# Kernel optimization log

Measured on AMD Instinct MI355X. Metric: run time of the kernel, lower is better.

Reference implementation:

```python
import jax, jax.numpy as jnp
import numpy as np
import math

B, S, D = 2, 1024, 2048
H, HD, ROT = 16, 128, 64
LQ, LKV = 1024, 512
ED, E, TOPK = 1024, 8, 2
EPS = 1e-6

def _rms(x, w):
    return w * (x * jax.lax.rsqrt(jnp.mean(x * x, axis=-1, keepdims=True) + EPS))

def _rope(x, cos, sin):
    # x: [B,S,H,R]; pairs are (even, odd) lanes, complex multiply expanded
    x0, x1 = x[..., 0::2], x[..., 1::2]
    c = cos[None, :, None, :]
    s = sin[None, :, None, :]
    out = jnp.stack([x0 * c - x1 * s, x0 * s + x1 * c], axis=-1)
    return out.reshape(x.shape)

def setup_inputs() -> dict:
    key = jax.random.key(0)
    ks = jax.random.split(key, 32)
    def rn(k, shape, fan):
        return jax.random.normal(k, shape, jnp.float32) / math.sqrt(fan)
    # RoPE tables
    theta = 10000.0 ** (-np.arange(0, ROT, 2, dtype=np.float32) / ROT)
    ang = np.arange(S, dtype=np.float32)[:, None] * theta[None, :]
    inp = {
        'x': jax.random.normal(ks[0], (B, S, D), jnp.float32),
        'freqs_cos': jnp.asarray(np.cos(ang)),
        'freqs_sin': jnp.asarray(np.sin(ang)),
        'w_norm1': jnp.ones((D,), jnp.float32),
        'w_lq': rn(ks[1], (D, LQ), D),
        'w_lkv': rn(ks[2], (D, LKV), D),
        'w_q': rn(ks[3], (LQ, H * HD), LQ),
        'w_k': rn(ks[4], (LKV, H * HD), LKV),
        'w_v': rn(ks[5], (LKV, H * HD), LKV),
        'w_qr': rn(ks[6], (LQ, H * ROT), LQ),
        'b_qr': jnp.zeros((H * ROT,), jnp.float32),
        'w_kr': rn(ks[7], (D, H * ROT), D),
        'b_kr': jnp.zeros((H * ROT,), jnp.float32),
        'w_o': rn(ks[8], (H * HD, D), H * HD),
        'b_o': jnp.zeros((D,), jnp.float32),
        'w_norm2': jnp.ones((D,), jnp.float32),
        'w_moe_norm': jnp.ones((D,), jnp.float32),
        'centroids': jax.random.normal(ks[9], (E, D), jnp.float32),
        'ws1': rn(ks[10], (D, ED), D),
        'bs1': jnp.zeros((ED,), jnp.float32),
        'ws2': rn(ks[11], (ED, D), ED),
        'bs2': jnp.zeros((D,), jnp.float32),
        'wr1': rn(ks[12], (E, D, ED), D),
        'br1': jnp.zeros((E, ED), jnp.float32),
        'wr2': rn(ks[13], (E, ED, D), ED),
        'br2': jnp.zeros((E, D), jnp.float32),
    }
    return inp

def reference(x, freqs_cos, freqs_sin, w_norm1, w_lq, w_lkv, w_q, w_k, w_v,
              w_qr, b_qr, w_kr, b_kr, w_o, b_o, w_norm2, w_moe_norm,
              centroids, ws1, bs1, ws2, bs2, wr1, br1, wr2, br2):
    # --- MLA attention with residual ---
    h = _rms(x, w_norm1)
    cq = h @ w_lq                      # [B,S,LQ]
    ckv = h @ w_lkv                    # [B,S,LKV]
    q = (cq @ w_q).reshape(B, S, H, HD)
    qr = _rope((cq @ w_qr + b_qr).reshape(B, S, H, ROT), freqs_cos, freqs_sin)
    k = (ckv @ w_k).reshape(B, S, H, HD)
    kr = _rope((h @ w_kr + b_kr).reshape(B, S, H, ROT), freqs_cos, freqs_sin)
    v = (ckv @ w_v).reshape(B, S, H, HD)
    qc = jnp.concatenate([q, qr], axis=-1)   # [B,S,H,HD+ROT]
    kc = jnp.concatenate([k, kr], axis=-1)
    scores = jnp.einsum('bqhd,bkhd->bhqk', qc, kc) / math.sqrt(HD + ROT)
    att = jax.nn.softmax(scores, axis=-1)
    o = jnp.einsum('bhqk,bkhd->bqhd', att, v).reshape(B, S, H * HD)
    x = x + (o @ w_o + b_o)
    # --- DeepSeekMoE (double RMSNorm per source) ---
    hn = _rms(_rms(x, w_norm2), w_moe_norm)
    shared = jax.nn.gelu((hn @ ws1 + bs1) @ ws2 + bs2, approximate=False)
    t = hn.reshape(-1, D)                      # [T,D], T=B*S
    aff = jax.nn.softmax(t @ centroids.T, axis=-1)  # [T,E]
    sc, idx = jax.lax.top_k(aff, TOPK)
    mask = jnp.zeros_like(aff).at[jnp.arange(t.shape[0])[:, None], idx].set(sc)
    mid = jnp.einsum('td,edf->tef', t, wr1) + br1          # [T,E,ED]
    out_e = jax.nn.gelu(jnp.einsum('tef,efd->ted', mid, wr2) + br2,
                        approximate=False)                  # [T,E,D]
    routed = jnp.einsum('te,ted->td', mask, out_e).reshape(B, S, D)
    return x + (hn + shared + routed)
```

## Files before the change

kernel.cpp:

```cpp
#include <hip/hip_runtime.h>
#include <math.h>

#define TT   2048
#define DM   2048
#define SEQ  1024
#define NH   16
#define NE   8
#define MB_  (1024*1024)
#define ATT_SCALE 0.07216878364870322f

typedef unsigned short u16;
typedef __attribute__((ext_vector_type(8))) short s8v;
typedef __attribute__((ext_vector_type(4))) float f4v;

__device__ __forceinline__ u16 f2bf(float f) {
  unsigned u = __builtin_bit_cast(unsigned, f);
  unsigned r = (u + 0x7fffu + ((u >> 16) & 1u)) >> 16;
  return (u16)r;
}
__device__ __forceinline__ float bf2f(u16 h) {
  return __builtin_bit_cast(float, (unsigned)h << 16);
}
__device__ __forceinline__ float gelu_f(float x) {
  return 0.5f * x * (1.0f + erff(x * 0.7071067811865476f));
}
__device__ __forceinline__ f4v mfma16(s8v a, s8v b, f4v c) {
  return __builtin_amdgcn_mfma_f32_16x16x32_bf16(a, b, c, 0, 0, 0);
}

__global__ __launch_bounds__(256) void tcast_k(const float* __restrict__ src,
                                               u16* __restrict__ dst, int R, int C) {
  __shared__ float tile[32][33];
  const size_t bofs = (size_t)blockIdx.z * R * C;
  src += bofs; dst += bofs;
  const int r0 = blockIdx.y * 32, c0 = blockIdx.x * 32;
  const int t = threadIdx.x;
  const int tr = t >> 3, tc4 = (t & 7) * 4;
  float4 v = *(const float4*)&src[(size_t)(r0 + tr) * C + c0 + tc4];
  tile[tr][tc4 + 0] = v.x; tile[tr][tc4 + 1] = v.y;
  tile[tr][tc4 + 2] = v.z; tile[tr][tc4 + 3] = v.w;
  __syncthreads();
  ushort4 o;
  o.x = f2bf(tile[tc4 + 0][tr]);
  o.y = f2bf(tile[tc4 + 1][tr]);
  o.z = f2bf(tile[tc4 + 2][tr]);
  o.w = f2bf(tile[tc4 + 3][tr]);
  *(ushort4*)&dst[(size_t)(c0 + tr) * R + r0 + tc4] = o;
}

__device__ __forceinline__ float block_sum(float v, float* red) {
#pragma unroll
  for (int m = 32; m; m >>= 1) v += __shfl_xor(v, m);
  __syncthreads();
  if ((threadIdx.x & 63) == 0) red[threadIdx.x >> 6] = v;
  __syncthreads();
  return red[0] + red[1] + red[2] + red[3];
}

__global__ __launch_bounds__(256) void rmsb_k(const float* __restrict__ x,
                                              const float* __restrict__ w,
                                              u16* __restrict__ out) {
  __shared__ float red[4];
  const int t = blockIdx.x, tid = threadIdx.x;
  const float* xr = x + (size_t)t * DM;
  float4 v0 = *(const float4*)&xr[tid * 4];
  float4 v1 = *(const float4*)&xr[1024 + tid * 4];
  float ss = v0.x*v0.x + v0.y*v0.y + v0.z*v0.z + v0.w*v0.w
           + v1.x*v1.x + v1.y*v1.y + v1.z*v1.z + v1.w*v1.w;
  float s = block_sum(ss, red);
  float r = rsqrtf(s * (1.0f / DM) + 1e-6f);
  float4 w0 = *(const float4*)&w[tid * 4];
  float4 w1 = *(const float4*)&w[1024 + tid * 4];
  u16* orow = out + (size_t)t * DM;
  ushort4 o0, o1;
  o0.x = f2bf(v0.x*r*w0.x); o0.y = f2bf(v0.y*r*w0.y);
  o0.z = f2bf(v0.z*r*w0.z); o0.w = f2bf(v0.w*r*w0.w);
  o1.x = f2bf(v1.x*r*w1.x); o1.y = f2bf(v1.y*r*w1.y);
  o1.z = f2bf(v1.z*r*w1.z); o1.w = f2bf(v1.w*r*w1.w);
  *(ushort4*)&orow[tid * 4] = o0;
  *(ushort4*)&orow[1024 + tid * 4] = o1;
}

__global__ __launch_bounds__(256) void rms2_k(const float* __restrict__ x,
                                              const float* __restrict__ w2,
                                              const float* __restrict__ wm,
                                              float* __restrict__ outf,
                                              u16* __restrict__ outb) {
  __shared__ float red[4];
  const int t = blockIdx.x, tid = threadIdx.x;
  const float* xr = x + (size_t)t * DM;
  float4 v0 = *(const float4*)&xr[tid * 4];
  float4 v1 = *(const float4*)&xr[1024 + tid * 4];
  float ss = v0.x*v0.x + v0.y*v0.y + v0.z*v0.z + v0.w*v0.w
           + v1.x*v1.x + v1.y*v1.y + v1.z*v1.z + v1.w*v1.w;
  float s1 = block_sum(ss, red);
  float r1 = rsqrtf(s1 * (1.0f / DM) + 1e-6f);
  float4 a0 = *(const float4*)&w2[tid * 4];
  float4 a1 = *(const float4*)&w2[1024 + tid * 4];
  float4 y0 = make_float4(v0.x*r1*a0.x, v0.y*r1*a0.y, v0.z*r1*a0.z, v0.w*r1*a0.w);
  float4 y1 = make_float4(v1.x*r1*a1.x, v1.y*r1*a1.y, v1.z*r1*a1.z, v1.w*r1*a1.w);
  float ss2 = y0.x*y0.x + y0.y*y0.y + y0.z*y0.z + y0.w*y0.w
            + y1.x*y1.x + y1.y*y1.y + y1.z*y1.z + y1.w*y1.w;
  float s2 = block_sum(ss2, red);
  float r2 = rsqrtf(s2 * (1.0f / DM) + 1e-6f);
  float4 b0 = *(const float4*)&wm[tid * 4];
  float4 b1 = *(const float4*)&wm[1024 + tid * 4];
  float4 z0 = make_float4(y0.x*r2*b0.x, y0.y*r2*b0.y, y0.z*r2*b0.z, y0.w*r2*b0.w);
  float4 z1 = make_float4(y1.x*r2*b1.x, y1.y*r2*b1.y, y1.z*r2*b1.z, y1.w*r2*b1.w);
  float* orow = outf + (size_t)t * DM;
  *(float4*)&orow[tid * 4] = z0;
  *(float4*)&orow[1024 + tid * 4] = z1;
  u16* brow = outb + (size_t)t * DM;
  ushort4 o0, o1;
  o0.x = f2bf(z0.x); o0.y = f2bf(z0.y); o0.z = f2bf(z0.z); o0.w = f2bf(z0.w);
  o1.x = f2bf(z1.x); o1.y = f2bf(z1.y); o1.z = f2bf(z1.z); o1.w = f2bf(z1.w);
  *(ushort4*)&brow[tid * 4] = o0;
  *(ushort4*)&brow[1024 + tid * 4] = o1;
}

template <int ACT, bool BIAS, bool RES, int OUT>
__global__ __launch_bounds__(256) void bgemm_k(const u16* __restrict__ A, int lda,
                                               const u16* __restrict__ Bt, int ldb,
                                               void* __restrict__ C, int ldc, int K,
                                               const float* __restrict__ bias,
                                               const float* __restrict__ res, int ldr) {
  __shared__ u16 As[128 * 64];
  __shared__ u16 Bs[128 * 64];
  const int tid = threadIdx.x;
  const int lane = tid & 63, w = tid >> 6;
  const int wr = w >> 1, wc = w & 1;
  const int l15 = lane & 15, l4 = lane >> 4;
  const int bm = blockIdx.y * 128, bn = blockIdx.x * 128;
  int srow[4], ssw[4], scol[4];
#pragma unroll
  for (int i = 0; i < 4; ++i) {
    int q = i * 256 + tid;
    int row = q >> 3, c = q & 7;
    srow[i] = row; scol[i] = c * 8;
    ssw[i] = row * 64 + ((c ^ (row & 7)) * 8);
  }
  f4v acc[4][4] = {};
  for (int k0 = 0; k0 < K; k0 += 64) {
    s8v ra[4], rb[4];
#pragma unroll
    for (int i = 0; i < 4; ++i) {
      ra[i] = *(const s8v*)(A + (size_t)(bm + srow[i]) * lda + k0 + scol[i]);
      rb[i] = *(const s8v*)(Bt + (size_t)(bn + srow[i]) * ldb + k0 + scol[i]);
    }
    __syncthreads();
#pragma unroll
    for (int i = 0; i < 4; ++i) {
      *(s8v*)(As + ssw[i]) = ra[i];
      *(s8v*)(Bs + ssw[i]) = rb[i];
    }
    __syncthreads();
#pragma unroll
    for (int kk = 0; kk < 2; ++kk) {
      s8v af[4], bfr[4];
#pragma unroll
      for (int m = 0; m < 4; ++m) {
        int row = wr * 64 + m * 16 + l15;
        int c = kk * 4 + l4;
        af[m] = *(const s8v*)(As + row * 64 + ((c ^ (row & 7)) * 8));
      }
#pragma unroll
      for (int n = 0; n < 4; ++n) {
        int row = wc * 64 + n * 16 + l15;
        int c = kk * 4 + l4;
        bfr[n] = *(const s8v*)(Bs + row * 64 + ((c ^ (row & 7)) * 8));
      }
#pragma unroll
      for (int m = 0; m < 4; ++m)
#pragma unroll
        for (int n = 0; n < 4; ++n)
          acc[m][n] = mfma16(af[m], bfr[n], acc[m][n]);
    }
  }
#pragma unroll
  for (int m = 0; m < 4; ++m) {
    const int row0 = bm + wr * 64 + m * 16 + l4 * 4;
#pragma unroll
    for (int n = 0; n < 4; ++n) {
      const int col = bn + wc * 64 + n * 16 + l15;
      f4v v = acc[m][n];
      float bv = BIAS ? bias[col] : 0.0f;
      if (OUT == 2) {
        ushort4 o;
        o.x = f2bf(v[0] + bv); o.y = f2bf(v[1] + bv);
        o.z = f2bf(v[2] + bv); o.w = f2bf(v[3] + bv);
        *(ushort4*)((u16*)C + (size_t)col * ldc + row0) = o;
      } else {
#pragma unroll
        for (int r = 0; r < 4; ++r) {
          float o = v[r] + bv;
          if (RES) o += res[(size_t)(row0 + r) * ldr + col];
          if (ACT == 1) o = gelu_f(o);
          if (OUT == 1) ((u16*)C)[(size_t)(row0 + r) * ldc + col] = f2bf(o);
          else          ((float*)C)[(size_t)(row0 + r) * ldc + col] = o;
        }
      }
    }
  }
}

template <bool GATHER, int ACT>
__global__ __launch_bounds__(256) void bgemm_grp_k(const u16* __restrict__ A, int lda,
                                                   const u16* __restrict__ BtAll, int K, int N,
                                                   u16* __restrict__ C,
                                                   const float* __restrict__ biasAll,
                                                   const int* __restrict__ counts,
                                                   const int* __restrict__ bases,
                                                   const int* __restrict__ entry_token) {
  const int e = blockIdx.z;
  const int cnt = counts[e];
  const int m0 = blockIdx.y * 128;
  if (m0 >= cnt) return;
  const int base = bases[e];
  const u16* Bt = BtAll + (size_t)e * K * N;
  const float* bias = biasAll + (size_t)e * N;
  __shared__ u16 As[128 * 64];
  __shared__ u16 Bs[128 * 64];
  const int tid = threadIdx.x;
  const int lane = tid & 63, w = tid >> 6;
  const int wr = w >> 1, wc = w & 1;
  const int l15 = lane & 15, l4 = lane >> 4;
  const int bn = blockIdx.x * 128;
  int arow[4], srow[4], ssw[4], scol[4];
#pragma unroll
  for (int i = 0; i < 4; ++i) {
    int q = i * 256 + tid;
    int row = q >> 3, c = q & 7;
    srow[i] = row; scol[i] = c * 8;
    ssw[i] = row * 64 + ((c ^ (row & 7)) * 8);
    int rr = m0 + row; if (rr >= cnt) rr = cnt - 1;
    arow[i] = GATHER ? entry_token[base + rr] : (base + rr);
  }
  f4v acc[4][4] = {};
  for (int k0 = 0; k0 < K; k0 += 64) {
    s8v ra[4], rb[4];
#pragma unroll
    for (int i = 0; i < 4; ++i) {
      ra[i] = *(const s8v*)(A + (size_t)arow[i] * lda + k0 + scol[i]);
      rb[i] = *(const s8v*)(Bt + (size_t)(bn + srow[i]) * K + k0 + scol[i]);
    }
    __syncthreads();
#pragma unroll
    for (int i = 0; i < 4; ++i) {
      *(s8v*)(As + ssw[i]) = ra[i];
      *(s8v*)(Bs + ssw[i]) = rb[i];
    }
    __syncthreads();
#pragma unroll
    for (int kk = 0; kk < 2; ++kk) {
      s8v af[4], bfr[4];
#pragma unroll
      for (int m = 0; m < 4; ++m) {
        int row = wr * 64 + m * 16 + l15;
        int c = kk * 4 + l4;
        af[m] = *(const s8v*)(As + row * 64 + ((c ^ (row & 7)) * 8));
      }
#pragma unroll
      for (int n = 0; n < 4; ++n) {
        int row = wc * 64 + n * 16 + l15;
        int c = kk * 4 + l4;
        bfr[n] = *(const s8v*)(Bs + row * 64 + ((c ^ (row & 7)) * 8));
      }
#pragma unroll
      for (int m = 0; m < 4; ++m)
#pragma unroll
        for (int n = 0; n < 4; ++n)
          acc[m][n] = mfma16(af[m], bfr[n], acc[m][n]);
    }
  }
#pragma unroll
  for (int m = 0; m < 4; ++m) {
    const int rl0 = m0 + wr * 64 + m * 16 + l4 * 4;
#pragma unroll
    for (int n = 0; n < 4; ++n) {
      const int col = bn + wc * 64 + n * 16 + l15;
      f4v v = acc[m][n];
      float bv = bias[col];
#pragma unroll
      for (int r = 0; r < 4; ++r) {
        const int rl = rl0 + r;
        if (rl < cnt) {
          float o = v[r] + bv;
          if (ACT == 1) o = gelu_f(o);
          C[(size_t)(base + rl) * N + col] = f2bf(o);
        }
      }
    }
  }
}

__global__ __launch_bounds__(256) void ropeb_k(u16* __restrict__ buf,
                                               const float* __restrict__ cosb,
                                               const float* __restrict__ sinb) {
  const int i = blockIdx.x * 256 + threadIdx.x;
  const int t = i >> 9;
  const int rem = i & 511;
  const int hh2 = rem >> 5, p = rem & 31;
  const int s = t & (SEQ - 1);
  const float c = cosb[s * 32 + p], sn = sinb[s * 32 + p];
  unsigned* ptr = (unsigned*)(buf + (size_t)t * 1024 + hh2 * 64 + p * 2);
  unsigned vv = *ptr;
  float x0 = bf2f((u16)(vv & 0xffffu)), x1 = bf2f((u16)(vv >> 16));
  float y0 = x0 * c - x1 * sn, y1 = x0 * sn + x1 * c;
  *ptr = (unsigned)f2bf(y0) | ((unsigned)f2bf(y1) << 16);
}

__global__ __launch_bounds__(256) void attnb_k(const u16* __restrict__ qb,
                                               const u16* __restrict__ qrb,
                                               const u16* __restrict__ kb,
                                               const u16* __restrict__ krb,
                                               const u16* __restrict__ vt,
                                               u16* __restrict__ ob) {
  __shared__ u16 Ks[32 * 200];
  __shared__ u16 Vs[128 * 40];
  __shared__ u16 Ps[4][16 * 40];
  const int tid = threadIdx.x, lane = tid & 63, w = tid >> 6;
  const int l15 = lane & 15, l4 = lane >> 4;
  const int hh = blockIdx.y, bb = blockIdx.z;
  const int tbase = bb * SEQ;
  const int q0 = blockIdx.x * 64 + w * 16;
  const int qtok = tbase + q0 + l15;
  s8v aq[6];
#pragma unroll
  for (int kc = 0; kc < 4; ++kc)
    aq[kc] = *(const s8v*)(qb + (size_t)qtok * 2048 + hh * 128 + kc * 32 + l4 * 8);
#pragma unroll
  for (int kc = 0; kc < 2; ++kc)
    aq[4 + kc] = *(const s8v*)(qrb + (size_t)qtok * 1024 + hh * 64 + kc * 32 + l4 * 8);
  f4v o[8] = {};
  float m_run[4] = {-1e30f, -1e30f, -1e30f, -1e30f};
  float l_run[4] = {0.f, 0.f, 0.f, 0.f};
  for (int kt = 0; kt < SEQ / 32; ++kt) {
    __syncthreads();
#pragma unroll
    for (int i = 0; i < 3; ++i) {
      int q = i * 256 + tid;
      int row = q / 24, c = q % 24;
      int tok = tbase + kt * 32 + row;
      s8v v;
      if (c < 16) v = *(const s8v*)(kb  + (size_t)tok * 2048 + hh * 128 + c * 8);
      else        v = *(const s8v*)(krb + (size_t)tok * 1024 + hh * 64 + (c - 16) * 8);
      *(s8v*)(Ks + row * 200 + c * 8) = v;
    }
#pragma unroll
    for (int i = 0; i < 2; ++i) {
      int q = i * 256 + tid;
      int row = q >> 2, c = q & 3;
      s8v v = *(const s8v*)(vt + (size_t)(hh * 128 + row) * 2048 + tbase + kt * 32 + c * 8);
      *(s8v*)(Vs + row * 40 + c * 8) = v;
    }
    __syncthreads();
    f4v s0 = {}, s1 = {};
#pragma unroll
    for (int kc = 0; kc < 6; ++kc) {
      s8v bk0 = *(const s8v*)(Ks + l15 * 200 + kc * 32 + l4 * 8);
      s8v bk1 = *(const s8v*)(Ks + (16 + l15) * 200 + kc * 32 + l4 * 8);
      s0 = mfma16(aq[kc], bk0, s0);
      s1 = mfma16(aq[kc], bk1, s1);
    }
    float scf[4];
#pragma unroll
    for (int r = 0; r < 4; ++r) {
      float a = s0[r] * ATT_SCALE, b = s1[r] * ATT_SCALE;
      float mt = fmaxf(a, b);
#pragma unroll
      for (int msk = 1; msk < 16; msk <<= 1) mt = fmaxf(mt, __shfl_xor(mt, msk));
      float mn = fmaxf(m_run[r], mt);
      float p0 = __expf(a - mn), p1 = __expf(b - mn);
      float rs = p0 + p1;
#pragma unroll
      for (int msk = 1; msk < 16; msk <<= 1) rs += __shfl_xor(rs, msk);
      float sc = __expf(m_run[r] - mn);
      l_run[r] = l_run[r] * sc + rs;
      m_run[r] = mn;
      scf[r] = sc;
      int rq = l4 * 4 + r;
      Ps[w][rq * 40 + l15] = f2bf(p0);
      Ps[w][rq * 40 + 16 + l15] = f2bf(p1);
    }
#pragma unroll
    for (int dt = 0; dt < 8; ++dt) {
      o[dt][0] *= scf[0]; o[dt][1] *= scf[1];
      o[dt][2] *= scf[2]; o[dt][3] *= scf[3];
    }
    s8v pa = *(const s8v*)(&Ps[w][l15 * 40 + l4 * 8]);
#pragma unroll
    for (int dt = 0; dt < 8; ++dt) {
      s8v bv = *(const s8v*)(Vs + (dt * 16 + l15) * 40 + l4 * 8);
      o[dt] = mfma16(pa, bv, o[dt]);
    }
  }
  float linv[4];
#pragma unroll
  for (int r = 0; r < 4; ++r) linv[r] = 1.0f / l_run[r];
#pragma unroll
  for (int dt = 0; dt < 8; ++dt)
#pragma unroll
    for (int r = 0; r < 4; ++r)
      ob[(size_t)(tbase + q0 + l4 * 4 + r) * 2048 + hh * 128 + dt * 16 + l15] =
          f2bf(o[dt][r] * linv[r]);
}

__global__ __launch_bounds__(256) void router_k(const float* __restrict__ hn,
                                                const float* __restrict__ cent,
                                                int* __restrict__ topk_idx,
                                                float* __restrict__ topk_w,
                                                int* __restrict__ pos,
                                                int* __restrict__ counts) {
  const int t = blockIdx.x, tid = threadIdx.x;
  float p[NE] = {};
  const float* xr = hn + (size_t)t * DM;
  for (int d = tid * 4; d < DM; d += 1024) {
    float4 xv = *(const float4*)&xr[d];
#pragma unroll
    for (int e = 0; e < NE; ++e) {
      float4 cv = *(const float4*)&cent[e * DM + d];
      p[e] += xv.x * cv.x + xv.y * cv.y + xv.z * cv.z + xv.w * cv.w;
    }
  }
  __shared__ float wred[NE][4];
#pragma unroll
  for (int e = 0; e < NE; ++e) {
    float v = p[e];
#pragma unroll
    for (int m = 32; m; m >>= 1) v += __shfl_xor(v, m);
    if ((tid & 63) == 0) wred[e][tid >> 6] = v;
  }
  __syncthreads();
  if (tid == 0) {
    float lg[NE], mx = -3.0e38f;
    for (int e = 0; e < NE; ++e) {
      lg[e] = wred[e][0] + wred[e][1] + wred[e][2] + wred[e][3];
      mx = fmaxf(mx, lg[e]);
    }
    float pe[NE], sum = 0.f;
    for (int e = 0; e < NE; ++e) { pe[e] = expf(lg[e] - mx); sum += pe[e]; }
    const float inv = 1.f / sum;
    int i0 = 0; float v0 = -1.f;
    for (int e = 0; e < NE; ++e) { float a = pe[e] * inv; if (a > v0) { v0 = a; i0 = e; } }
    int i1 = 0; float v1 = -1.f;
    for (int e = 0; e < NE; ++e) { if (e == i0) continue; float a = pe[e] * inv; if (a > v1) { v1 = a; i1 = e; } }
    topk_idx[t * 2 + 0] = i0;
    topk_idx[t * 2 + 1] = i1;
    topk_w[t * 2 + 0] = v0;
    topk_w[t * 2 + 1] = v1;
    pos[t * 2 + 0] = atomicAdd(&counts[i0], 1);
    pos[t * 2 + 1] = atomicAdd(&counts[i1], 1);
  }
}

__global__ __launch_bounds__(256) void scatter_k(const int* __restrict__ topk_idx,
                                                 const int* __restrict__ pos,
                                                 const int* __restrict__ counts,
                                                 int* __restrict__ bases,
                                                 int* __restrict__ entry_token,
                                                 int* __restrict__ token_entry) {
  __shared__ int sb[NE];
  const int tid = threadIdx.x;
  if (tid == 0) {
    int acc = 0;
    for (int e = 0; e < NE; ++e) { sb[e] = acc; bases[e] = acc; acc += counts[e]; }
  }
  __syncthreads();
  for (int i = tid; i < TT * 2; i += 256) {
    const int e = topk_idx[i];
    const int entry = sb[e] + pos[i];
    entry_token[entry] = i >> 1;
    token_entry[i] = entry;
  }
}

__global__ __launch_bounds__(256) void combine_k(const float* __restrict__ x2,
                                                 const float* __restrict__ hn,
                                                 const float* __restrict__ sh,
                                                 const u16* __restrict__ oute,
                                                 const int* __restrict__ token_entry,
                                                 const float* __restrict__ topk_w,
                                                 float* __restrict__ out) {
  const int i = blockIdx.x * 256 + threadIdx.x;
  const int t = i >> 9;
  const int c = (i & 511) * 4;
  const int e0 = token_entry[t * 2 + 0], e1 = token_entry[t * 2 + 1];
  const float w0 = topk_w[t * 2 + 0], w1 = topk_w[t * 2 + 1];
  float4 a = *(const float4*)&x2[(size_t)t * DM + c];
  float4 b = *(const float4*)&hn[(size_t)t * DM + c];
  float4 s = *(const float4*)&sh[(size_t)t * DM + c];
  ushort4 u0 = *(const ushort4*)&oute[(size_t)e0 * DM + c];
  ushort4 u1 = *(const ushort4*)&oute[(size_t)e1 * DM + c];
  *(float4*)&out[(size_t)t * DM + c] =
      make_float4(a.x + b.x + s.x + w0 * bf2f(u0.x) + w1 * bf2f(u1.x),
                  a.y + b.y + s.y + w0 * bf2f(u0.y) + w1 * bf2f(u1.y),
                  a.z + b.z + s.z + w0 * bf2f(u0.z) + w1 * bf2f(u1.z),
                  a.w + b.w + s.w + w0 * bf2f(u0.w) + w1 * bf2f(u1.w));
}

extern "C" void kernel_launch(void* const* d_in, const int* in_sizes, int n_in,
                              void* d_out, int out_size, void* d_ws, size_t ws_size,
                              hipStream_t stream) {
  (void)in_sizes; (void)n_in; (void)out_size; (void)ws_size;
  const float* x       = (const float*)d_in[0];
  const float* fc      = (const float*)d_in[1];
  const float* fs      = (const float*)d_in[2];
  const float* w_norm1 = (const float*)d_in[3];
  const float* w_lq    = (const float*)d_in[4];
  const float* w_lkv   = (const float*)d_in[5];
  const float* w_q     = (const float*)d_in[6];
  const float* w_k     = (const float*)d_in[7];
  const float* w_v     = (const float*)d_in[8];
  const float* w_qr    = (const float*)d_in[9];
  const float* b_qr    = (const float*)d_in[10];
  const float* w_kr    = (const float*)d_in[11];
  const float* b_kr    = (const float*)d_in[12];
  const float* w_o     = (const float*)d_in[13];
  const float* b_o     = (const float*)d_in[14];
  const float* w_norm2 = (const float*)d_in[15];
  const float* w_moe   = (const float*)d_in[16];
  const float* cent    = (const float*)d_in[17];
  const float* ws1     = (const float*)d_in[18];
  const float* bs1     = (const float*)d_in[19];
  const float* ws2     = (const float*)d_in[20];
  const float* bs2     = (const float*)d_in[21];
  const float* wr1     = (const float*)d_in[22];
  const float* br1     = (const float*)d_in[23];
  const float* wr2     = (const float*)d_in[24];
  const float* br2     = (const float*)d_in[25];
  float* out = (float*)d_out;

  char* W = (char*)d_ws;
  u16* wt_lq  = (u16*)(W + (size_t)0  * MB_);
  u16* wt_lkv = (u16*)(W + (size_t)4  * MB_);
  u16* wt_q   = (u16*)(W + (size_t)6  * MB_);
  u16* wt_qr  = (u16*)(W + (size_t)10 * MB_);
  u16* wt_k   = (u16*)(W + (size_t)12 * MB_);
  u16* wt_kr  = (u16*)(W + (size_t)14 * MB_);
  u16* wt_v   = (u16*)(W + (size_t)18 * MB_);
  u16* wt_o   = (u16*)(W + (size_t)20 * MB_);
  u16* wt_s1  = (u16*)(W + (size_t)28 * MB_);
  u16* wt_s2  = (u16*)(W + (size_t)32 * MB_);
  u16* wt_r1  = (u16*)(W + (size_t)36 * MB_);
  u16* wt_r2  = (u16*)(W + (size_t)68 * MB_);
  u16* h_bf   = (u16*)(W + (size_t)100 * MB_);
  u16* cq_bf  = (u16*)(W + (size_t)108 * MB_);
  u16* ckv_bf = (u16*)(W + (size_t)112 * MB_);
  u16* qbuf   = (u16*)(W + (size_t)114 * MB_);
  u16* qrbuf  = (u16*)(W + (size_t)122 * MB_);
  u16* kbuf   = (u16*)(W + (size_t)126 * MB_);
  u16* krbuf  = (u16*)(W + (size_t)134 * MB_);
  u16* vbuf_t = (u16*)(W + (size_t)138 * MB_);
  u16* obuf   = (u16*)(W + (size_t)146 * MB_);
  float* x2   = (float*)(W + (size_t)100 * MB_);
  float* hn   = (float*)(W + (size_t)116 * MB_);
  u16* hn_bf  = (u16*)(W + (size_t)132 * MB_);
  u16* s1b    = (u16*)(W + (size_t)140 * MB_);
  float* shb  = (float*)(W + (size_t)144 * MB_);
  u16* midb   = (u16*)(W + (size_t)160 * MB_);
  u16* oute   = (u16*)(W + (size_t)168 * MB_);
  int* ip          = (int*)(W + (size_t)184 * MB_);
  int* counts      = ip;
  int* bases       = ip + 8;
  int* topk_idx    = ip + 16;
  int* pos         = ip + 16 + 4096;
  int* token_entry = ip + 16 + 8192;
  int* entry_token = ip + 16 + 12288;
  float* topk_w    = (float*)(ip + 16 + 16384);

  tcast_k<<<dim3(32, 64), 256, 0, stream>>>(w_lq,  wt_lq,  2048, 1024);
  tcast_k<<<dim3(16, 64), 256, 0, stream>>>(w_lkv, wt_lkv, 2048, 512);
  tcast_k<<<dim3(64, 32), 256, 0, stream>>>(w_q,   wt_q,   1024, 2048);
  tcast_k<<<dim3(32, 32), 256, 0, stream>>>(w_qr,  wt_qr,  1024, 1024);
  tcast_k<<<dim3(64, 16), 256, 0, stream>>>(w_k,   wt_k,   512,  2048);
  tcast_k<<<dim3(32, 64), 256, 0, stream>>>(w_kr,  wt_kr,  2048, 1024);
  tcast_k<<<dim3(64, 16), 256, 0, stream>>>(w_v,   wt_v,   512,  2048);
  tcast_k<<<dim3(64, 64), 256, 0, stream>>>(w_o,   wt_o,   2048, 2048);
  tcast_k<<<dim3(32, 64), 256, 0, stream>>>(ws1,   wt_s1,  2048, 1024);
  tcast_k<<<dim3(64, 32), 256, 0, stream>>>(ws2,   wt_s2,  1024, 2048);
  tcast_k<<<dim3(32, 64, 8), 256, 0, stream>>>(wr1, wt_r1, 2048, 1024);
  tcast_k<<<dim3(64, 32, 8), 256, 0, stream>>>(wr2, wt_r2, 1024, 2048);

  rmsb_k<<<TT, 256, 0, stream>>>(x, w_norm1, h_bf);
  bgemm_k<0, false, false, 1><<<dim3(8, 16), 256, 0, stream>>>(h_bf, 2048, wt_lq, 2048, cq_bf, 1024, 2048, nullptr, nullptr, 0);
  bgemm_k<0, false, false, 1><<<dim3(4, 16), 256, 0, stream>>>(h_bf, 2048, wt_lkv, 2048, ckv_bf, 512, 2048, nullptr, nullptr, 0);
  bgemm_k<0, false, false, 1><<<dim3(16, 16), 256, 0, stream>>>(cq_bf, 1024, wt_q, 1024, qbuf, 2048, 1024, nullptr, nullptr, 0);
  bgemm_k<0, true,  false, 1><<<dim3(8, 16), 256, 0, stream>>>(cq_bf, 1024, wt_qr, 1024, qrbuf, 1024, 1024, b_qr, nullptr, 0);
  bgemm_k<0, false, false, 1><<<dim3(16, 16), 256, 0, stream>>>(ckv_bf, 512, wt_k, 512, kbuf, 2048, 512, nullptr, nullptr, 0);
  bgemm_k<0, true,  false, 1><<<dim3(8, 16), 256, 0, stream>>>(h_bf, 2048, wt_kr, 2048, krbuf, 1024, 2048, b_kr, nullptr, 0);
  bgemm_k<0, false, false, 2><<<dim3(16, 16), 256, 0, stream>>>(ckv_bf, 512, wt_v, 512, vbuf_t, 2048, 512, nullptr, nullptr, 0);
  ropeb_k<<<4096, 256, 0, stream>>>(qrbuf, fc, fs);
  ropeb_k<<<4096, 256, 0, stream>>>(krbuf, fc, fs);
  attnb_k<<<dim3(16, NH, 2), 256, 0, stream>>>(qbuf, qrbuf, kbuf, krbuf, vbuf_t, obuf);
  bgemm_k<0, true, true, 0><<<dim3(16, 16), 256, 0, stream>>>(obuf, 2048, wt_o, 2048, x2, 2048, 2048, b_o, x, 2048);
  rms2_k<<<TT, 256, 0, stream>>>(x2, w_norm2, w_moe, hn, hn_bf);
  bgemm_k<0, true, false, 1><<<dim3(8, 16), 256, 0, stream>>>(hn_bf, 2048, wt_s1, 2048, s1b, 1024, 2048, bs1, nullptr, 0);
  bgemm_k<1, true, false, 0><<<dim3(16, 16), 256, 0, stream>>>(s1b, 1024, wt_s2, 1024, shb, 2048, 1024, bs2, nullptr, 0);
  hipMemsetAsync(counts, 0, NE * sizeof(int), stream);
  router_k<<<TT, 256, 0, stream>>>(hn, cent, topk_idx, topk_w, pos, counts);
  scatter_k<<<1, 256, 0, stream>>>(topk_idx, pos, counts, bases, entry_token, token_entry);
  bgemm_grp_k<true, 0><<<dim3(8, 32, NE), 256, 0, stream>>>(hn_bf, 2048, wt_r1, 2048, 1024, midb, br1, counts, bases, entry_token);
  bgemm_grp_k<false, 1><<<dim3(16, 32, NE), 256, 0, stream>>>(midb, 1024, wt_r2, 1024, 2048, oute, br2, counts, bases, nullptr);
  combine_k<<<4096, 256, 0, stream>>>(x2, hn, shb, oute, token_entry, topk_w, out);
}
```

Measured before the change: 905.0 us.

## Fuse attention projection GEMMs and load GEMM tiles directly into LDS

The separate projections that share an input are merged into wider GEMMs by concatenating transposed weights: lq, lkv and kr share one GEMM on h, q and qr share one on cq, and k and v share one on ckv, with v written transposed through a split epilogue. Bias vectors are packed into combined buffers by a small fill kernel. GEMM operand tiles are now staged with global_load_lds, bypassing registers, and the XOR swizzle on the LDS layout is dropped. Launch count and tail waves drop, but the unswizzled LDS reads may cause bank conflicts, and loads are still not double-buffered.

```diff
diff --git a/kernel.cpp b/kernel.cpp
--- a/kernel.cpp
+++ b/kernel.cpp
@@ -26,6 +26,11 @@
 }
 __device__ __forceinline__ f4v mfma16(s8v a, s8v b, f4v c) {
   return __builtin_amdgcn_mfma_f32_16x16x32_bf16(a, b, c, 0, 0, 0);
+}
+__device__ __forceinline__ void gload16(const u16* g, u16* l) {
+  __builtin_amdgcn_global_load_lds(
+      (const __attribute__((address_space(1))) unsigned*)g,
+      (__attribute__((address_space(3))) unsigned*)l, 16, 0, 0);
 }
 
 __global__ __launch_bounds__(256) void tcast_k(const float* __restrict__ src,
@@ -46,6 +51,15 @@
   o.z = f2bf(tile[tc4 + 2][tr]);
   o.w = f2bf(tile[tc4 + 3][tr]);
   *(ushort4*)&dst[(size_t)(c0 + tr) * R + r0 + tc4] = o;
+}
+
+__global__ __launch_bounds__(256) void biasfill_k(float* __restrict__ bh,
+                                                  float* __restrict__ bq,
+                                                  const float* __restrict__ bkr,
+                                                  const float* __restrict__ bqr) {
+  const int i = blockIdx.x * 256 + threadIdx.x;
+  if (i < 2560) bh[i] = (i >= 1536) ? bkr[i - 1536] : 0.f;
+  bq[i] = (i >= 2048) ? bqr[i - 2048] : 0.f;
 }
 
 __device__ __forceinline__ float block_sum(float v, float* red) {
@@ -123,7 +137,8 @@
                                                const u16* __restrict__ Bt, int ldb,
                                                void* __restrict__ C, int ldc, int K,
                                                const float* __restrict__ bias,
-                                               const float* __restrict__ res, int ldr) {
+                                               const float* __restrict__ res, int ldr,
+                                               void* __restrict__ C2, int ldc2, int nsplit) {
   __shared__ u16 As[128 * 64];
   __shared__ u16 Bs[128 * 64];
   const int tid = threadIdx.x;
@@ -131,44 +146,29 @@
   const int wr = w >> 1, wc = w & 1;
   const int l15 = lane & 15, l4 = lane >> 4;
   const int bm = blockIdx.y * 128, bn = blockIdx.x * 128;
-  int srow[4], ssw[4], scol[4];
-#pragma unroll
-  for (int i = 0; i < 4; ++i) {
-    int q = i * 256 + tid;
-    int row = q >> 3, c = q & 7;
-    srow[i] = row; scol[i] = c * 8;
-    ssw[i] = row * 64 + ((c ^ (row & 7)) * 8);
-  }
+  const int lrow = lane >> 3, lcol = (lane & 7) * 8;
+  const u16* Abase = A + (size_t)(bm + w * 32 + lrow) * lda + lcol;
+  const u16* Bbase = Bt + (size_t)(bn + w * 32 + lrow) * ldb + lcol;
+  u16* AsW = As + (w * 32) * 64;
+  u16* BsW = Bs + (w * 32) * 64;
   f4v acc[4][4] = {};
   for (int k0 = 0; k0 < K; k0 += 64) {
-    s8v ra[4], rb[4];
-#pragma unroll
-    for (int i = 0; i < 4; ++i) {
-      ra[i] = *(const s8v*)(A + (size_t)(bm + srow[i]) * lda + k0 + scol[i]);
-      rb[i] = *(const s8v*)(Bt + (size_t)(bn + srow[i]) * ldb + k0 + scol[i]);
-    }
     __syncthreads();
 #pragma unroll
-    for (int i = 0; i < 4; ++i) {
-      *(s8v*)(As + ssw[i]) = ra[i];
-      *(s8v*)(Bs + ssw[i]) = rb[i];
+    for (int j = 0; j < 4; ++j) {
+      gload16(Abase + (size_t)j * 8 * lda + k0, AsW + j * 8 * 64);
+      gload16(Bbase + (size_t)j * 8 * ldb + k0, BsW + j * 8 * 64);
     }
     __syncthreads();
 #pragma unroll
     for (int kk = 0; kk < 2; ++kk) {
       s8v af[4], bfr[4];
 #pragma unroll
-      for (int m = 0; m < 4; ++m) {
-        int row = wr * 64 + m * 16 + l15;
-        int c = kk * 4 + l4;
-        af[m] = *(const s8v*)(As + row * 64 + ((c ^ (row & 7)) * 8));
-      }
-#pragma unroll
-      for (int n = 0; n < 4; ++n) {
-        int row = wc * 64 + n * 16 + l15;
-        int c = kk * 4 + l4;
-        bfr[n] = *(const s8v*)(Bs + row * 64 + ((c ^ (row & 7)) * 8));
-      }
+      for (int m = 0; m < 4; ++m)
+        af[m] = *(const s8v*)(As + (wr * 64 + m * 16 + l15) * 64 + kk * 32 + l4 * 8);
+#pragma unroll
+      for (int n = 0; n < 4; ++n)
+        bfr[n] = *(const s8v*)(Bs + (wc * 64 + n * 16 + l15) * 64 + kk * 32 + l4 * 8);
 #pragma unroll
       for (int m = 0; m < 4; ++m)
 #pragma unroll
@@ -184,19 +184,19 @@
       const int col = bn + wc * 64 + n * 16 + l15;
       f4v v = acc[m][n];
       float bv = BIAS ? bias[col] : 0.0f;
-      if (OUT == 2) {
+      if (OUT == 3 && col >= nsplit) {
         ushort4 o;
         o.x = f2bf(v[0] + bv); o.y = f2bf(v[1] + bv);
         o.z = f2bf(v[2] + bv); o.w = f2bf(v[3] + bv);
-        *(ushort4*)((u16*)C + (size_t)col * ldc + row0) = o;
+        *(ushort4*)((u16*)C2 + (size_t)(col - nsplit) * ldc2 + row0) = o;
       } else {
 #pragma unroll
         for (int r = 0; r < 4; ++r) {
           float o = v[r] + bv;
           if (RES) o += res[(size_t)(row0 + r) * ldr + col];
           if (ACT == 1) o = gelu_f(o);
-          if (OUT == 1) ((u16*)C)[(size_t)(row0 + r) * ldc + col] = f2bf(o);
-          else          ((float*)C)[(size_t)(row0 + r) * ldc + col] = o;
+          if (OUT == 0) ((float*)C)[(size_t)(row0 + r) * ldc + col] = o;
+          else          ((u16*)C)[(size_t)(row0 + r) * ldc + col] = f2bf(o);
         }
       }
     }
@@ -225,46 +225,35 @@
   const int wr = w >> 1, wc = w & 1;
   const int l15 = lane & 15, l4 = lane >> 4;
   const int bn = blockIdx.x * 128;
-  int arow[4], srow[4], ssw[4], scol[4];
-#pragma unroll
-  for (int i = 0; i < 4; ++i) {
-    int q = i * 256 + tid;
-    int row = q >> 3, c = q & 7;
-    srow[i] = row; scol[i] = c * 8;
-    ssw[i] = row * 64 + ((c ^ (row & 7)) * 8);
-    int rr = m0 + row; if (rr >= cnt) rr = cnt - 1;
-    arow[i] = GATHER ? entry_token[base + rr] : (base + rr);
-  }
+  const int lrow = lane >> 3, lcol = (lane & 7) * 8;
+  int aro[4];
+#pragma unroll
+  for (int j = 0; j < 4; ++j) {
+    int rr = m0 + w * 32 + j * 8 + lrow;
+    if (rr >= cnt) rr = cnt - 1;
+    aro[j] = GATHER ? entry_token[base + rr] : (base + rr);
+  }
+  const u16* Bbase = Bt + (size_t)(bn + w * 32 + lrow) * K + lcol;
+  u16* AsW = As + (w * 32) * 64;
+  u16* BsW = Bs + (w * 32) * 64;
   f4v acc[4][4] = {};
   for (int k0 = 0; k0 < K; k0 += 64) {
-    s8v ra[4], rb[4];
-#pragma unroll
-    for (int i = 0; i < 4; ++i) {
-      ra[i] = *(const s8v*)(A + (size_t)arow[i] * lda + k0 + scol[i]);
-      rb[i] = *(const s8v*)(Bt + (size_t)(bn + srow[i]) * K + k0 + scol[i]);
-    }
     __syncthreads();
 #pragma unroll
-    for (int i = 0; i < 4; ++i) {
-      *(s8v*)(As + ssw[i]) = ra[i];
-      *(s8v*)(Bs + ssw[i]) = rb[i];
+    for (int j = 0; j < 4; ++j) {
+      gload16(A + (size_t)aro[j] * lda + k0 + lcol, AsW + j * 8 * 64);
+      gload16(Bbase + (size_t)j * 8 * K + k0, BsW + j * 8 * 64);
     }
     __syncthreads();
 #pragma unroll
     for (int kk = 0; kk < 2; ++kk) {
       s8v af[4], bfr[4];
 #pragma unroll
-      for (int m = 0; m < 4; ++m) {
-        int row = wr * 64 + m * 16 + l15;
-        int c = kk * 4 + l4;
-        af[m] = *(const s8v*)(As + row * 64 + ((c ^ (row & 7)) * 8));
-      }
-#pragma unroll
-      for (int n = 0; n < 4; ++n) {
-        int row = wc * 64 + n * 16 + l15;
-        int c = kk * 4 + l4;
-        bfr[n] = *(const s8v*)(Bs + row * 64 + ((c ^ (row & 7)) * 8));
-      }
+      for (int m = 0; m < 4; ++m)
+        af[m] = *(const s8v*)(As + (wr * 64 + m * 16 + l15) * 64 + kk * 32 + l4 * 8);
+#pragma unroll
+      for (int n = 0; n < 4; ++n)
+        bfr[n] = *(const s8v*)(Bs + (wc * 64 + n * 16 + l15) * 64 + kk * 32 + l4 * 8);
 #pragma unroll
       for (int m = 0; m < 4; ++m)
 #pragma unroll
@@ -293,7 +282,7 @@
   }
 }
 
-__global__ __launch_bounds__(256) void ropeb_k(u16* __restrict__ buf,
+__global__ __launch_bounds__(256) void ropeb_k(u16* __restrict__ buf, int ldb,
                                                const float* __restrict__ cosb,
                                                const float* __restrict__ sinb) {
   const int i = blockIdx.x * 256 + threadIdx.x;
@@ -302,17 +291,17 @@
   const int hh2 = rem >> 5, p = rem & 31;
   const int s = t & (SEQ - 1);
   const float c = cosb[s * 32 + p], sn = sinb[s * 32 + p];
-  unsigned* ptr = (unsigned*)(buf + (size_t)t * 1024 + hh2 * 64 + p * 2);
+  unsigned* ptr = (unsigned*)(buf + (size_t)t * ldb + hh2 * 64 + p * 2);
   unsigned vv = *ptr;
   float x0 = bf2f((u16)(vv & 0xffffu)), x1 = bf2f((u16)(vv >> 16));
   float y0 = x0 * c - x1 * sn, y1 = x0 * sn + x1 * c;
   *ptr = (unsigned)f2bf(y0) | ((unsigned)f2bf(y1) << 16);
 }
 
-__global__ __launch_bounds__(256) void attnb_k(const u16* __restrict__ qb,
-                                               const u16* __restrict__ qrb,
-                                               const u16* __restrict__ kb,
-                                               const u16* __restrict__ krb,
+__global__ __launch_bounds__(256) void attnb_k(const u16* __restrict__ qb, int ldq,
+                                               const u16* __restrict__ qrb, int ldqr,
+                                               const u16* __restrict__ kb, int ldk,
+                                               const u16* __restrict__ krb, int ldkr,
                                                const u16* __restrict__ vt,
                                                u16* __restrict__ ob) {
   __shared__ u16 Ks[32 * 200];
@@ -327,10 +316,10 @@
   s8v aq[6];
 #pragma unroll
   for (int kc = 0; kc < 4; ++kc)
-    aq[kc] = *(const s8v*)(qb + (size_t)qtok * 2048 + hh * 128 + kc * 32 + l4 * 8);
+    aq[kc] = *(const s8v*)(qb + (size_t)qtok * ldq + hh * 128 + kc * 32 + l4 * 8);
 #pragma unroll
   for (int kc = 0; kc < 2; ++kc)
-    aq[4 + kc] = *(const s8v*)(qrb + (size_t)qtok * 1024 + hh * 64 + kc * 32 + l4 * 8);
+    aq[4 + kc] = *(const s8v*)(qrb + (size_t)qtok * ldqr + hh * 64 + kc * 32 + l4 * 8);
   f4v o[8] = {};
   float m_run[4] = {-1e30f, -1e30f, -1e30f, -1e30f};
   float l_run[4] = {0.f, 0.f, 0.f, 0.f};
@@ -342,8 +331,8 @@
       int row = q / 24, c = q % 24;
       int tok = tbase + kt * 32 + row;
       s8v v;
-      if (c < 16) v = *(const s8v*)(kb  + (size_t)tok * 2048 + hh * 128 + c * 8);
-      else        v = *(const s8v*)(krb + (size_t)tok * 1024 + hh * 64 + (c - 16) * 8);
+      if (c < 16) v = *(const s8v*)(kb  + (size_t)tok * ldk + hh * 128 + c * 8);
+      else        v = *(const s8v*)(krb + (size_t)tok * ldkr + hh * 64 + (c - 16) * 8);
       *(s8v*)(Ks + row * 200 + c * 8) = v;
     }
 #pragma unroll
@@ -531,25 +520,18 @@
   float* out = (float*)d_out;
 
   char* W = (char*)d_ws;
-  u16* wt_lq  = (u16*)(W + (size_t)0  * MB_);
-  u16* wt_lkv = (u16*)(W + (size_t)4  * MB_);
-  u16* wt_q   = (u16*)(W + (size_t)6  * MB_);
-  u16* wt_qr  = (u16*)(W + (size_t)10 * MB_);
-  u16* wt_k   = (u16*)(W + (size_t)12 * MB_);
-  u16* wt_kr  = (u16*)(W + (size_t)14 * MB_);
-  u16* wt_v   = (u16*)(W + (size_t)18 * MB_);
+  u16* wt_h   = (u16*)(W + (size_t)0  * MB_);
+  u16* wt_qqr = (u16*)(W + (size_t)10 * MB_);
+  u16* wt_kv  = (u16*)(W + (size_t)16 * MB_);
   u16* wt_o   = (u16*)(W + (size_t)20 * MB_);
   u16* wt_s1  = (u16*)(W + (size_t)28 * MB_);
   u16* wt_s2  = (u16*)(W + (size_t)32 * MB_);
   u16* wt_r1  = (u16*)(W + (size_t)36 * MB_);
   u16* wt_r2  = (u16*)(W + (size_t)68 * MB_);
   u16* h_bf   = (u16*)(W + (size_t)100 * MB_);
-  u16* cq_bf  = (u16*)(W + (size_t)108 * MB_);
-  u16* ckv_bf = (u16*)(W + (size_t)112 * MB_);
-  u16* qbuf   = (u16*)(W + (size_t)114 * MB_);
-  u16* qrbuf  = (u16*)(W + (size_t)122 * MB_);
-  u16* kbuf   = (u16*)(W + (size_t)126 * MB_);
-  u16* krbuf  = (u16*)(W + (size_t)134 * MB_);
+  u16* hp     = (u16*)(W + (size_t)108 * MB_);
+  u16* qp     = (u16*)(W + (size_t)118 * MB_);
+  u16* kbuf   = (u16*)(W + (size_t)130 * MB_);
   u16* vbuf_t = (u16*)(W + (size_t)138 * MB_);
   u16* obuf   = (u16*)(W + (size_t)146 * MB_);
   float* x2   = (float*)(W + (size_t)100 * MB_);
@@ -567,39 +549,47 @@
   int* token_entry = ip + 16 + 8192;
   int* entry_token = ip + 16 + 12288;
   float* topk_w    = (float*)(ip + 16 + 16384);
-
-  tcast_k<<<dim3(32, 64), 256, 0, stream>>>(w_lq,  wt_lq,  2048, 1024);
-  tcast_k<<<dim3(16, 64), 256, 0, stream>>>(w_lkv, wt_lkv, 2048, 512);
-  tcast_k<<<dim3(64, 32), 256, 0, stream>>>(w_q,   wt_q,   1024, 2048);
-  tcast_k<<<dim3(32, 32), 256, 0, stream>>>(w_qr,  wt_qr,  1024, 1024);
-  tcast_k<<<dim3(64, 16), 256, 0, stream>>>(w_k,   wt_k,   512,  2048);
-  tcast_k<<<dim3(32, 64), 256, 0, stream>>>(w_kr,  wt_kr,  2048, 1024);
-  tcast_k<<<dim3(64, 16), 256, 0, stream>>>(w_v,   wt_v,   512,  2048);
-  tcast_k<<<dim3(64, 64), 256, 0, stream>>>(w_o,   wt_o,   2048, 2048);
-  tcast_k<<<dim3(32, 64), 256, 0, stream>>>(ws1,   wt_s1,  2048, 1024);
-  tcast_k<<<dim3(64, 32), 256, 0, stream>>>(ws2,   wt_s2,  1024, 2048);
-  tcast_k<<<dim3(32, 64, 8), 256, 0, stream>>>(wr1, wt_r1, 2048, 1024);
-  tcast_k<<<dim3(64, 32, 8), 256, 0, stream>>>(wr2, wt_r2, 1024, 2048);
+  float* bias_h    = (float*)(ip + 16 + 20480);
+  float* bias_q    = bias_h + 2560;
+
+  tcast_k<<<dim3(32, 64), 256, 0, stream>>>(w_lq,  wt_h,                    2048, 1024);
+  tcast_k<<<dim3(16, 64), 256, 0, stream>>>(w_lkv, wt_h + 1024 * 2048,      2048, 512);
+  tcast_k<<<dim3(32, 64), 256, 0, stream>>>(w_kr,  wt_h + 1536 * 2048,      2048, 1024);
+  tcast_k<<<dim3(64, 32), 256, 0, stream>>>(w_q,   wt_qqr,                  1024, 2048);
+  tcast_k<<<dim3(32, 32), 256, 0, stream>>>(w_qr,  wt_qqr + 2048 * 1024,    1024, 1024);
+  tcast_k<<<dim3(64, 16), 256, 0, stream>>>(w_k,   wt_kv,                   512,  2048);
+  tcast_k<<<dim3(64, 16), 256, 0, stream>>>(w_v,   wt_kv + 2048 * 512,      512,  2048);
+  tcast_k<<<dim3(64, 64), 256, 0, stream>>>(w_o,   wt_o,                    2048, 2048);
+  tcast_k<<<dim3(32, 64), 256, 0, stream>>>(ws1,   wt_s1,                   2048, 1024);
+  tcast_k<<<dim3(64, 32), 256, 0, stream>>>(ws2,   wt_s2,                   1024, 2048);
+  tcast_k<<<dim3(32, 64, 8), 256, 0, stream>>>(wr1, wt_r1,                  2048, 1024);
+  tcast_k<<<dim3(64, 32, 8), 256, 0, stream>>>(wr2, wt_r2,                  1024, 2048);
+  biasfill_k<<<12, 256, 0, stream>>>(bias_h, bias_q, b_kr, b_qr);
 
   rmsb_k<<<TT, 256, 0, stream>>>(x, w_norm1, h_bf);
-  bgemm_k<0, false, false, 1><<<dim3(8, 16), 256, 0, stream>>>(h_bf, 2048, wt_lq, 2048, cq_bf, 1024, 2048, nullptr, nullptr, 0);
-  bgemm_k<0, false, false, 1><<<dim3(4, 16), 256, 0, stream>>>(h_bf, 2048, wt_lkv, 2048, ckv_bf, 512, 2048, nullptr, nullptr, 0);
-  bgemm_k<0, false, false, 1><<<dim3(16, 16), 256, 0, stream>>>(cq_bf, 1024, wt_q, 1024, qbuf, 2048, 1024, nullptr, nullptr, 0);
-  bgemm_k<0, true,  false, 1><<<dim3(8, 16), 256, 0, stream>>>(cq_bf, 1024, wt_qr, 1024, qrbuf, 1024, 1024, b_qr, nullptr, 0);
-  bgemm_k<0, false, false, 1><<<dim3(16, 16), 256, 0, stream>>>(ckv_bf, 512, wt_k, 512, kbuf, 2048, 512, nullptr, nullptr, 0);
-  bgemm_k<0, true,  false, 1><<<dim3(8, 16), 256, 0, stream>>>(h_bf, 2048, wt_kr, 2048, krbuf, 1024, 2048, b_kr, nullptr, 0);
-  bgemm_k<0, false, false, 2><<<dim3(16, 16), 256, 0, stream>>>(ckv_bf, 512, wt_v, 512, vbuf_t, 2048, 512, nullptr, nullptr, 0);
-  ropeb_k<<<4096, 256, 0, stream>>>(qrbuf, fc, fs);
-  ropeb_k<<<4096, 256, 0, stream>>>(krbuf, fc, fs);
-  attnb_k<<<dim3(16, NH, 2), 256, 0, stream>>>(qbuf, qrbuf, kbuf, krbuf, vbuf_t, obuf);
-  bgemm_k<0, true, true, 0><<<dim3(16, 16), 256, 0, stream>>>(obuf, 2048, wt_o, 2048, x2, 2048, 2048, b_o, x, 2048);
+  bgemm_k<0, true, false, 1><<<dim3(20, 16), 256, 0, stream>>>(
+      h_bf, 2048, wt_h, 2048, hp, 2560, 2048, bias_h, nullptr, 0, nullptr, 0, 0);
+  bgemm_k<0, true, false, 1><<<dim3(24, 16), 256, 0, stream>>>(
+      hp, 2560, wt_qqr, 1024, qp, 3072, 1024, bias_q, nullptr, 0, nullptr, 0, 0);
+  bgemm_k<0, false, false, 3><<<dim3(32, 16), 256, 0, stream>>>(
+      hp + 1024, 2560, wt_kv, 512, kbuf, 2048, 512, nullptr, nullptr, 0, vbuf_t, 2048, 2048);
+  ropeb_k<<<4096, 256, 0, stream>>>(qp + 2048, 3072, fc, fs);
+  ropeb_k<<<4096, 256, 0, stream>>>(hp + 1536, 2560, fc, fs);
+  attnb_k<<<dim3(16, NH, 2), 256, 0, stream>>>(qp, 3072, qp + 2048, 3072,
+                                               kbuf, 2048, hp + 1536, 2560, vbuf_t, obuf);
+  bgemm_k<0, true, true, 0><<<dim3(16, 16), 256, 0, stream>>>(
+      obuf, 2048, wt_o, 2048, x2, 2048, 2048, b_o, x, 2048, nullptr, 0, 0);
   rms2_k<<<TT, 256, 0, stream>>>(x2, w_norm2, w_moe, hn, hn_bf);
-  bgemm_k<0, true, false, 1><<<dim3(8, 16), 256, 0, stream>>>(hn_bf, 2048, wt_s1, 2048, s1b, 1024, 2048, bs1, nullptr, 0);
-  bgemm_k<1, true, false, 0><<<dim3(16, 16), 256, 0, stream>>>(s1b, 1024, wt_s2, 1024, shb, 2048, 1024, bs2, nullptr, 0);
+  bgemm_k<0, true, false, 1><<<dim3(8, 16), 256, 0, stream>>>(
+      hn_bf, 2048, wt_s1, 2048, s1b, 1024, 2048, bs1, nullptr, 0, nullptr, 0, 0);
+  bgemm_k<1, true, false, 0><<<dim3(16, 16), 256, 0, stream>>>(
+      s1b, 1024, wt_s2, 1024, shb, 2048, 1024, bs2, nullptr, 0, nullptr, 0, 0);
   hipMemsetAsync(counts, 0, NE * sizeof(int), stream);
   router_k<<<TT, 256, 0, stream>>>(hn, cent, topk_idx, topk_w, pos, counts);
   scatter_k<<<1, 256, 0, stream>>>(topk_idx, pos, counts, bases, entry_token, token_entry);
-  bgemm_grp_k<true, 0><<<dim3(8, 32, NE), 256, 0, stream>>>(hn_bf, 2048, wt_r1, 2048, 1024, midb, br1, counts, bases, entry_token);
-  bgemm_grp_k<false, 1><<<dim3(16, 32, NE), 256, 0, stream>>>(midb, 1024, wt_r2, 1024, 2048, oute, br2, counts, bases, nullptr);
+  bgemm_grp_k<true, 0><<<dim3(8, 32, NE), 256, 0, stream>>>(
+      hn_bf, 2048, wt_r1, 2048, 1024, midb, br1, counts, bases, entry_token);
+  bgemm_grp_k<false, 1><<<dim3(16, 32, NE), 256, 0, stream>>>(
+      midb, 1024, wt_r2, 1024, 2048, oute, br2, counts, bases, nullptr);
   combine_k<<<4096, 256, 0, stream>>>(x2, hn, shb, oute, token_entry, topk_w, out);
 }
```

Measured after the change: 847.9 us. 6.3% less time.
